# Optimization experiments

Hardware: AMD Instinct MI355X
Metric: run time of the kernel (lower is better)

## Reference

```python
import jax, jax.numpy as jnp
import numpy as np

SIGMA = 16.0


def setup_inputs() -> dict:
    key = jax.random.key(0)
    k1, k2, k3 = jax.random.split(key, 3)
    B, T, D = 8, 2048, 1024
    x = jax.random.normal(k1, (B, T, D), dtype=jnp.float32)
    posv = jax.random.randint(k2, (B, T), 0, 64, dtype=jnp.int32)
    posh = jax.random.randint(k3, (B, T), 0, 64, dtype=jnp.int32)
    return {"x": x, "posv": posv, "posh": posh}


def reference(x, posv, posh):
    # pos: [B, T, 2] float, as in torch.stack([posv, posh], -1).float()
    pos = jnp.stack([posv, posh], axis=-1).astype(jnp.float32)
    # pairwise squared distances: [B, T, T]
    diff = pos[:, :, None, :] - pos[:, None, :, :]
    dist_sq = jnp.sum(diff * diff, axis=-1)
    kernel = jnp.exp(-dist_sq / (2.0 * SIGMA * SIGMA))
    kernel = kernel / jnp.sum(kernel, axis=-1, keepdims=True)
    # dropout is identity in eval mode
    return jnp.einsum("bts,bsd->btd", kernel, x)
```

## Files before the change

kernel.cpp:

```cpp
#include <hip/hip_runtime.h>
#include <hip/hip_bf16.h>

#define NB 8
#define NT 2048
#define ND 1024
#define CAP 2048

typedef unsigned short ushort_t;
using short8 = __attribute__((ext_vector_type(8))) short;
using f32x4  = __attribute__((ext_vector_type(4))) float;

__device__ __forceinline__ ushort_t f2bf(float f) {
    __hip_bfloat16 h = __float2bfloat16(f);
    return *reinterpret_cast<ushort_t*>(&h);
}
__device__ __forceinline__ float bf2f(ushort_t u) {
    unsigned int v = ((unsigned int)u) << 16;
    return __int_as_float((int)v);
}

__device__ __forceinline__ int xcd_swizzle() {
    int bid = (int)blockIdx.x;
    return (bid >> 3) + ((bid & 7) * ((int)gridDim.x >> 3));
}


#define OFF_G2     256
#define OFF_AFH    768
#define OFF_AFL    8960
#define OFF_CNTV   17152
#define OFF_CNTH   19200
#define OFF_INVDEN 21248
#define OFF_GOFF   152320
#define OFF_TOKV   160512
#define OFF_TOKH   4354816
#define OFF_TOKV2  8549120
#define OFF_B1     12743424
#define B1_SLAB    ((size_t)64 * 64 * 1024 * 2)

__device__ __forceinline__ void kden_body(
    int kb, const int* __restrict__ posv, const int* __restrict__ posh,
    float* __restrict__ invden, int b0)
{
    int b   = b0 + (kb >> 3);
    int phg = kb & 7;
    int tid = threadIdx.x;

    __shared__ int   hist[64][64];
    __shared__ float g2s[128];
    __shared__ float tmp[64][8];

#pragma unroll
    for (int k = 0; k < 16; k++) ((int*)hist)[tid + (k << 8)] = 0;
    if (tid < 128) {
        int k = tid, r = k - 63;
        g2s[tid] = (k < 127) ? expf(-(float)(r * r) * (1.0f / 512.0f)) : 0.0f;
    }
    __syncthreads();
#pragma unroll
    for (int k = 0; k < 8; k++) {
        int t = (k << 8) + tid;
        atomicAdd(&hist[posv[b * NT + t]][posh[b * NT + t]], 1);
    }
    __syncthreads();
#pragma unroll
    for (int c = 0; c < 2; c++) {
        int cell = (c << 8) + tid;
        int j    = cell >> 3;
        int phl  = cell & 7;
        int ph   = (phg << 3) + phl;
        float s = 0.f;
        for (int k = 0; k < 64; k++)
            s += (float)hist[j][k] * g2s[63 + k - ph];
        tmp[j][phl] = s;
    }
    __syncthreads();
#pragma unroll
    for (int c = 0; c < 2; c++) {
        int cell = (c << 8) + tid;
        int pv   = cell >> 3;
        int phl  = cell & 7;
        int ph   = (phg << 3) + phl;
        float s = 0.f;
        for (int j = 0; j < 64; j++)
            s += g2s[63 + j - pv] * tmp[j][phl];
        invden[(b * 64 + pv) * 64 + ph] = 1.0f / s;
    }
}

__global__ __launch_bounds__(256) void k1_bucket(
    const int* __restrict__ posv, const int* __restrict__ posh,
    int* __restrict__ tokv2, int4* __restrict__ goff,
    int* __restrict__ tokh,
    int* __restrict__ cntv, int* __restrict__ cnth,
    float* __restrict__ gbase, ushort_t* __restrict__ AfH,
    ushort_t* __restrict__ AfL, float* __restrict__ invden, int nbkt)
{
    if ((int)blockIdx.x >= nbkt) {
        kden_body((int)blockIdx.x - nbkt, posv, posh, invden, 0);
        return;
    }

    int b    = blockIdx.x >> 5;
    int blk  = blockIdx.x & 31;
    int wave = threadIdx.x >> 6;
    int lane = threadIdx.x & 63;

    if (blockIdx.x == 0) {
        if (threadIdx.x < 192) {
            int k = (int)threadIdx.x - 64;
            float v = 0.0f;
            if (k >= 0 && k < 127) {
                int r = k - 63;
                v = expf(-(float)(r * r) * (1.0f / 512.0f));
            }
            gbase[threadIdx.x] = v;
        }
#pragma unroll
        for (int p = 0; p < 16; p++) {
            int pos = (p << 8) + (int)threadIdx.x;
            int i   = pos & 7;
            int ln  = (pos >> 3) & 63;
            int ks  = (pos >> 9) & 1;
            int w   = pos >> 10;
            int q   = (w << 4) + (ln & 15);
            int k   = (ks << 5) + ((i >> 2) << 4) + ((ln >> 4) << 2) + (i & 3);
            int dlt = q - k;
            float g = expf(-(float)(dlt * dlt) * (1.0f / 512.0f));
            ushort_t hi = f2bf(g);
            AfH[pos] = hi;
            AfL[pos] = f2bf(g - bf2f(hi));
        }
    }

    int task   = blk * 4 + wave;
    int bucket = task & 63;
    int use_ph = task >> 6;
    int bkt    = b * 64 + bucket;

    int comb[32];
#pragma unroll
    for (int k = 0; k < 32; k++) {
        int t = k * 64 + lane;
        comb[k] = posv[b * NT + t] | (posh[b * NT + t] << 16);
    }

    unsigned long long lmask = (1ull << lane) - 1ull;

    if (use_ph == 0) {
        int* dst = tokv2 + (size_t)bkt * CAP;
        int cg0 = 0, cg1 = 0, cg2 = 0, cg3 = 0;
#pragma unroll 4
        for (int k = 0; k < 32; k++) {
            bool hit = (comb[k] & 0xffff) == bucket;
            int grp = (comb[k] >> 20) & 3;
            cg0 += (int)__popcll(__ballot(hit && grp == 0));
            cg1 += (int)__popcll(__ballot(hit && grp == 1));
            cg2 += (int)__popcll(__ballot(hit && grp == 2));
            cg3 += (int)__popcll(__ballot(hit && grp == 3));
        }
        int s1 = cg0, s2 = cg0 + cg1, s3 = cg0 + cg1 + cg2;
        int tot = s3 + cg3;
        if (lane == 0) {
            goff[bkt] = make_int4(0, s1, s2, s3);
            cntv[bkt] = tot;
        }
        int c0 = 0, c1 = s1, c2 = s2, c3 = s3;
#pragma unroll 4
        for (int k = 0; k < 32; k++) {
            bool hit = (comb[k] & 0xffff) == bucket;
            int grp = (comb[k] >> 20) & 3;
            unsigned long long m0 = __ballot(hit && grp == 0);
            unsigned long long m1 = __ballot(hit && grp == 1);
            unsigned long long m2 = __ballot(hit && grp == 2);
            unsigned long long m3 = __ballot(hit && grp == 3);
            if (hit) {
                int p;
                if      (grp == 0) p = c0 + (int)__popcll(m0 & lmask);
                else if (grp == 1) p = c1 + (int)__popcll(m1 & lmask);
                else if (grp == 2) p = c2 + (int)__popcll(m2 & lmask);
                else               p = c3 + (int)__popcll(m3 & lmask);
                dst[p] = (k * 64 + lane) | (comb[k] & 0xffff0000);
            }
            c0 += (int)__popcll(m0); c1 += (int)__popcll(m1);
            c2 += (int)__popcll(m2); c3 += (int)__popcll(m3);
        }
    } else {
        int* dst = tokh + (size_t)bkt * CAP;
        int cursor = 0;
#pragma unroll 4
        for (int k = 0; k < 32; k++) {
            bool hit = ((comb[k] >> 16) == bucket);
            unsigned long long m = __ballot(hit);
            if (hit)
                dst[cursor + __popcll(m & lmask)] =
                    (k * 64 + lane) | ((comb[k] & 0xffff) << 16);
            cursor += (int)__popcll(m);
        }
        if (lane == 0) cnth[bkt] = cursor;
    }
}

__global__ __launch_bounds__(256) void kden(
    const int* __restrict__ posv, const int* __restrict__ posh,
    float* __restrict__ invden, int b0)
{
    kden_body((int)blockIdx.x, posv, posh, invden, b0);
}

__device__ __forceinline__ short8 ldsBfrag(const ushort_t* rowp, int ks, int g4) {
    const ushort_t* p = rowp + (ks << 5) + g4;
    uint2 lo = *(const uint2*)(p);
    uint2 hi = *(const uint2*)(p + 16);
    uint4 pk; pk.x = lo.x; pk.y = lo.y; pk.z = hi.x; pk.w = hi.y;
    return __builtin_bit_cast(short8, pk);
}

__global__ __launch_bounds__(256) void k2_convh(
    const float* __restrict__ x,
    const int* __restrict__ tokv2, const int* __restrict__ cntv,
    const int4* __restrict__ goff,
    const ushort_t* __restrict__ AfH, const ushort_t* __restrict__ AfL,
    ushort_t* __restrict__ B1, int b0)
{
    int ell  = xcd_swizzle();
    int dc   = ell & 15;
    int pv   = (ell >> 4) & 63;
    int b    = b0 + (ell >> 10);
    int tid  = threadIdx.x;
    int lane = tid & 63;
    int w    = tid >> 6;
    int d0   = dc << 6;

    __shared__ float ldsf[64 * 65];
    float    (*S)[65]   = (float(*)[65])ldsf;
    ushort_t (*S16)[68] = (ushort_t(*)[68])ldsf;

    int bucket = (b << 6) + pv;
    int n = cntv[bucket];
    const int* toks = tokv2 + (size_t)bucket * CAP;
    const float* xb = x + (((size_t)b * NT) << 10) + d0 + lane;

    int4 go = goff[bucket];
    int gs = (w == 0) ? go.x : (w == 1) ? go.y : (w == 2) ? go.z : go.w;
    int ge = (w == 3) ? n   : (w == 0) ? go.y : (w == 1) ? go.z : go.w;

    int wn0 = ge - gs; if (wn0 < 0) wn0 = 0; if (wn0 > 64) wn0 = 64;
    int m0  = wn0 > 8 ? 8 : wn0;
    int m1  = wn0 > 8 ? (wn0 > 16 ? 8 : wn0 - 8) : 0;
    int pkv = (wn0 > 0) ? toks[gs + lane] : 0;
    int pk0[8], pk1[8]; float xv0[8], xv1[8];
#pragma unroll
    for (int j = 0; j < 8; j++) pk0[j] = __builtin_amdgcn_readlane(pkv, j);
#pragma unroll
    for (int j = 0; j < 8; j++)
        if (j < m0) xv0[j] = xb[(size_t)(pk0[j] & 0xffff) << 10];
#pragma unroll
    for (int j = 0; j < 8; j++) pk1[j] = __builtin_amdgcn_readlane(pkv, 8 + j);
#pragma unroll
    for (int j = 0; j < 8; j++)
        if (j < m1) xv1[j] = xb[(size_t)(pk1[j] & 0xffff) << 10];

    short8 ahi[2], alo[2];
#pragma unroll
    for (int ks = 0; ks < 2; ks++) {
        int idx = ((((w << 1) + ks) << 6) + lane) << 3;
        ahi[ks] = *(const short8*)(AfH + idx);
        alo[ks] = *(const short8*)(AfL + idx);
    }

#pragma unroll
    for (int k = 0; k < 17; k++) {
        int idx = (k << 8) + tid;
        if (idx < 64 * 65) ldsf[idx] = 0.f;
    }
    __syncthreads();

#pragma unroll
    for (int j = 0; j < 8; j++)
        if (j < m0) S[lane][pk0[j] >> 16] += xv0[j];
#pragma unroll
    for (int j = 0; j < 8; j++)
        if (j < m1) S[lane][pk1[j] >> 16] += xv1[j];

    for (int i = 16; i < wn0; i += 8) {
        int m = wn0 - i; if (m > 8) m = 8;
        int pk[8]; float xv[8];
#pragma unroll
        for (int j = 0; j < 8; j++) pk[j] = __builtin_amdgcn_readlane(pkv, i + j);
#pragma unroll
        for (int j = 0; j < 8; j++)
            if (j < m) xv[j] = xb[(size_t)(pk[j] & 0xffff) << 10];
#pragma unroll
        for (int j = 0; j < 8; j++)
            if (j < m) S[lane][pk[j] >> 16] += xv[j];
    }
    for (int win = gs + 64; win < ge; win += 64) {
        int wn = ge - win; if (wn > 64) wn = 64;
        int pkw = toks[win + lane];
        for (int i = 0; i < wn; i += 8) {
            int m = wn - i; if (m > 8) m = 8;
            int pk[8]; float xv[8];
#pragma unroll
            for (int j = 0; j < 8; j++) pk[j] = __builtin_amdgcn_readlane(pkw, i + j);
#pragma unroll
            for (int j = 0; j < 8; j++)
                if (j < m) xv[j] = xb[(size_t)(pk[j] & 0xffff) << 10];
#pragma unroll
            for (int j = 0; j < 8; j++)
                if (j < m) S[lane][pk[j] >> 16] += xv[j];
        }
    }
    __syncthreads();

    {
        int r  = tid & 63;
        int c0 = (tid >> 6) << 4;
        float vals[16];
#pragma unroll
        for (int c = 0; c < 16; c++) vals[c] = S[r][c0 + c];
        __syncthreads();
#pragma unroll
        for (int c = 0; c < 16; c++) S16[r][c0 + c] = f2bf(vals[c]);
    }
    __syncthreads();

    int g4 = (lane >> 4) << 2;
    int qbase = (w << 4) + g4;

    f32x4 accs[4];
#pragma unroll
    for (int nt = 0; nt < 4; nt++) {
        const ushort_t* rowp = &S16[(nt << 4) + (lane & 15)][0];
        f32x4 a = {0.f, 0.f, 0.f, 0.f};
#pragma unroll
        for (int ks = 0; ks < 2; ks++) {
            short8 bf = ldsBfrag(rowp, ks, g4);
            a = __builtin_amdgcn_mfma_f32_16x16x32_bf16(ahi[ks], bf, a, 0, 0, 0);
            a = __builtin_amdgcn_mfma_f32_16x16x32_bf16(alo[ks], bf, a, 0, 0, 0);
        }
        accs[nt] = a;
    }
    __syncthreads();

#pragma unroll
    for (int nt = 0; nt < 4; nt++)
#pragma unroll
        for (int reg = 0; reg < 4; reg++)
            S16[qbase + reg][(nt << 4) + (lane & 15)] = f2bf(accs[nt][reg]);
    __syncthreads();

    ushort_t* B1p = B1 + (((size_t)(b - b0)) << 22) + (((size_t)pv) << 10) + d0;
#pragma unroll
    for (int pass = 0; pass < 2; pass++) {
        int row = (pass << 5) + (tid >> 3);
        int col = (tid & 7) << 3;
        uint4 v = *(const uint4*)(&S16[row][col]);
        *reinterpret_cast<uint4*>(B1p + ((size_t)row << 16) + col) = v;
    }
}

__global__ __launch_bounds__(256) void k3_convv(
    const int* __restrict__ tokh, const int* __restrict__ cnth,
    const ushort_t* __restrict__ AfH, const ushort_t* __restrict__ AfL,
    const ushort_t* __restrict__ B1, const float* __restrict__ invden,
    float* __restrict__ out, int b0)
{
    int ell  = xcd_swizzle();
    int dc   = ell & 15;
    int ph   = (ell >> 4) & 63;
    int b    = b0 + (ell >> 10);
    int tid  = threadIdx.x;
    int lane = tid & 63;
    int w    = tid >> 6;
    int d0   = dc << 6;

    int n = cnth[(b << 6) + ph];
    if (n == 0) return;

    __shared__ float ldsf[64 * 65];
    ushort_t (*u16)[68] = (ushort_t(*)[68])ldsf;
    float    (*y)[65]   = (float(*)[65])ldsf;

    const ushort_t* B1b = B1 + (((size_t)(b - b0)) << 22) + (((size_t)ph) << 16)
                        + d0 + lane;
#pragma unroll
    for (int it = 0; it < 16; it++) {
        int j = (w << 4) + it;
        u16[lane][j] = B1b[(size_t)j << 10];
    }
    __syncthreads();

    short8 ahi[2], alo[2];
#pragma unroll
    for (int ks = 0; ks < 2; ks++) {
        int idx = ((((w << 1) + ks) << 6) + lane) << 3;
        ahi[ks] = *(const short8*)(AfH + idx);
        alo[ks] = *(const short8*)(AfL + idx);
    }
    int g4 = (lane >> 4) << 2;
    int qbase = (w << 4) + g4;

    f32x4 accs[4];
#pragma unroll
    for (int nt = 0; nt < 4; nt++) {
        const ushort_t* rowp = &u16[(nt << 4) + (lane & 15)][0];
        f32x4 a = {0.f, 0.f, 0.f, 0.f};
#pragma unroll
        for (int ks = 0; ks < 2; ks++) {
            short8 bf = ldsBfrag(rowp, ks, g4);
            a = __builtin_amdgcn_mfma_f32_16x16x32_bf16(ahi[ks], bf, a, 0, 0, 0);
            a = __builtin_amdgcn_mfma_f32_16x16x32_bf16(alo[ks], bf, a, 0, 0, 0);
        }
        accs[nt] = a;
    }
    __syncthreads();

#pragma unroll
    for (int nt = 0; nt < 4; nt++)
#pragma unroll
        for (int reg = 0; reg < 4; reg++)
            y[qbase + reg][(nt << 4) + (lane & 15)] = accs[nt][reg];
    __syncthreads();

    const int* toks = tokh + ((size_t)((b << 6) + ph)) * CAP;
    float* outb = out + (((size_t)b * NT) << 10) + d0 + lane;
    const float* ivb = invden + ((b << 6) << 6) + ph;

    int nch = (n + 3) >> 2;
    for (int c = w; c < nch; c += 4) {
        int i0 = c << 2;
        int4 M = *(const int4*)(toks + i0);
        int pk[4];
        pk[0] = __builtin_amdgcn_readfirstlane(M.x);
        pk[1] = __builtin_amdgcn_readfirstlane(M.y);
        pk[2] = __builtin_amdgcn_readfirstlane(M.z);
        pk[3] = __builtin_amdgcn_readfirstlane(M.w);
#pragma unroll
        for (int j = 0; j < 4; j++) {
            if (i0 + j < n) {
                int t   = pk[j] & 0xffff;
                int pvt = pk[j] >> 16;
                float iv = ivb[pvt << 6];
                outb[(size_t)t << 10] = y[pvt][lane] * iv;
            }
        }
    }
}

__global__ __launch_bounds__(256) void k_naive(
    const float* __restrict__ x, const int* __restrict__ posv,
    const int* __restrict__ posh, float* __restrict__ out)
{
    int t   = blockIdx.x & (NT - 1);
    int b   = blockIdx.x >> 11;
    int tid = threadIdx.x;

    __shared__ float s_w[NT];
    __shared__ float s_red[256];

    int pvt = posv[b * NT + t];
    int pht = posh[b * NT + t];

    float dsum = 0.0f;
    for (int s = tid; s < NT; s += 256) {
        int dv = pvt - posv[b * NT + s];
        int dh = pht - posh[b * NT + s];
        float w = expf(-(float)(dv * dv + dh * dh) * (1.0f / 512.0f));
        s_w[s] = w;
        dsum += w;
    }
    s_red[tid] = dsum;
    __syncthreads();
    for (int off = 128; off > 0; off >>= 1) {
        if (tid < off) s_red[tid] += s_red[tid + off];
        __syncthreads();
    }
    float inv = 1.0f / s_red[0];

    float a0 = 0.f, a1 = 0.f, a2 = 0.f, a3 = 0.f;
    for (int s = 0; s < NT; s++) {
        float w = s_w[s];
        const float* xr = x + (((size_t)(b * NT + s)) << 10);
        a0 = fmaf(w, xr[tid + 0],   a0);
        a1 = fmaf(w, xr[tid + 256], a1);
        a2 = fmaf(w, xr[tid + 512], a2);
        a3 = fmaf(w, xr[tid + 768], a3);
    }
    size_t ob = (((size_t)(b * NT + t)) << 10) + tid;
    out[ob + 0]   = a0 * inv;
    out[ob + 256] = a1 * inv;
    out[ob + 512] = a2 * inv;
    out[ob + 768] = a3 * inv;
}

extern "C" void kernel_launch(void* const* d_in, const int* in_sizes, int n_in,
                              void* d_out, int out_size, void* d_ws, size_t ws_size,
                              hipStream_t stream) {
    const float* x    = (const float*)d_in[0];
    const int*   posv = (const int*)d_in[1];
    const int*   posh = (const int*)d_in[2];
    float*       out  = (float*)d_out;

    char* ws = (char*)d_ws;
    float*    gbase  = (float*)ws;
    ushort_t* AfH    = (ushort_t*)(ws + OFF_AFH);
    ushort_t* AfL    = (ushort_t*)(ws + OFF_AFL);
    int*      cntv   = (int*)(ws + OFF_CNTV);
    int*      cnth   = (int*)(ws + OFF_CNTH);
    float*    invden = (float*)(ws + OFF_INVDEN);
    int4*     goff   = (int4*)(ws + OFF_GOFF);
    int*      tokh   = (int*)(ws + OFF_TOKH);
    int*      tokv2  = (int*)(ws + OFF_TOKV2);
    ushort_t* B1     = (ushort_t*)(ws + OFF_B1);

    const size_t needFull = (size_t)OFF_B1 + (size_t)NB * B1_SLAB;
    const size_t needLoop = (size_t)OFF_B1 + B1_SLAB;

    if (ws_size >= needFull) {
        k1_bucket<<<NB * 32 + NB * 8, 256, 0, stream>>>(
            posv, posh, tokv2, goff, tokh, cntv, cnth, gbase, AfH, AfL,
            invden, NB * 32);
        k2_convh<<<NB * 1024, 256, 0, stream>>>(x, tokv2, cntv, goff, AfH, AfL, B1, 0);
        k3_convv<<<NB * 1024, 256, 0, stream>>>(tokh, cnth, AfH, AfL, B1, invden, out, 0);
    } else if (ws_size >= needLoop) {
        k1_bucket<<<NB * 32, 256, 0, stream>>>(
            posv, posh, tokv2, goff, tokh, cntv, cnth, gbase, AfH, AfL,
            invden, NB * 32);
        for (int b = 0; b < NB; b++) {
            kden<<<8, 256, 0, stream>>>(posv, posh, invden, b);
            k2_convh<<<1024, 256, 0, stream>>>(x, tokv2, cntv, goff, AfH, AfL, B1, b);
            k3_convv<<<1024, 256, 0, stream>>>(tokh, cnth, AfH, AfL, B1, invden, out, b);
        }
    } else {
        k_naive<<<NB * NT, 256, 0, stream>>>(x, posv, posh, out);
    }
}
```

Measured before the change: 72.07 us.

## Process two position buckets per k2_convh block with prefetch overlap

Each k2_convh block now handles two consecutive posv buckets instead of one, halving the grid. The first gather batch of the second bucket is issued before the first bucket's MFMA and store phase, so its global loads overlap with that work. This reuses the A-fragment loads across both buckets and cuts block launch overhead. In exchange there are fewer blocks to hide latency, more registers in use, and extra barriers inside each block.

```diff
diff --git a/kernel.cpp b/kernel.cpp
--- a/kernel.cpp
+++ b/kernel.cpp
@@ -225,8 +225,8 @@
 {
     int ell  = xcd_swizzle();
     int dc   = ell & 15;
-    int pv   = (ell >> 4) & 63;
-    int b    = b0 + (ell >> 10);
+    int pp   = (ell >> 4) & 31;
+    int b    = b0 + (ell >> 9);
     int tid  = threadIdx.x;
     int lane = tid & 63;
     int w    = tid >> 6;
@@ -236,30 +236,9 @@
     float    (*S)[65]   = (float(*)[65])ldsf;
     ushort_t (*S16)[68] = (ushort_t(*)[68])ldsf;
 
-    int bucket = (b << 6) + pv;
-    int n = cntv[bucket];
-    const int* toks = tokv2 + (size_t)bucket * CAP;
     const float* xb = x + (((size_t)b * NT) << 10) + d0 + lane;
 
-    int4 go = goff[bucket];
-    int gs = (w == 0) ? go.x : (w == 1) ? go.y : (w == 2) ? go.z : go.w;
-    int ge = (w == 3) ? n   : (w == 0) ? go.y : (w == 1) ? go.z : go.w;
-
-    int wn0 = ge - gs; if (wn0 < 0) wn0 = 0; if (wn0 > 64) wn0 = 64;
-    int m0  = wn0 > 8 ? 8 : wn0;
-    int m1  = wn0 > 8 ? (wn0 > 16 ? 8 : wn0 - 8) : 0;
-    int pkv = (wn0 > 0) ? toks[gs + lane] : 0;
-    int pk0[8], pk1[8]; float xv0[8], xv1[8];
-#pragma unroll
-    for (int j = 0; j < 8; j++) pk0[j] = __builtin_amdgcn_readlane(pkv, j);
-#pragma unroll
-    for (int j = 0; j < 8; j++)
-        if (j < m0) xv0[j] = xb[(size_t)(pk0[j] & 0xffff) << 10];
-#pragma unroll
-    for (int j = 0; j < 8; j++) pk1[j] = __builtin_amdgcn_readlane(pkv, 8 + j);
-#pragma unroll
-    for (int j = 0; j < 8; j++)
-        if (j < m1) xv1[j] = xb[(size_t)(pk1[j] & 0xffff) << 10];
+    int bucket0 = (b << 6) + (pp << 1);
 
     short8 ahi[2], alo[2];
 #pragma unroll
@@ -268,6 +247,29 @@
         ahi[ks] = *(const short8*)(AfH + idx);
         alo[ks] = *(const short8*)(AfL + idx);
     }
+    int g4 = (lane >> 4) << 2;
+    int qbase = (w << 4) + g4;
+
+    int n0 = cntv[bucket0];
+    const int* toks0 = tokv2 + (size_t)bucket0 * CAP;
+    int4 go0 = goff[bucket0];
+    int gs0 = (w == 0) ? go0.x : (w == 1) ? go0.y : (w == 2) ? go0.z : go0.w;
+    int ge0 = (w == 3) ? n0  : (w == 0) ? go0.y : (w == 1) ? go0.z : go0.w;
+    int wn0 = ge0 - gs0; if (wn0 < 0) wn0 = 0; if (wn0 > 64) wn0 = 64;
+    int m00 = wn0 > 8 ? 8 : wn0;
+    int m01 = wn0 > 8 ? (wn0 > 16 ? 8 : wn0 - 8) : 0;
+    int pkv0 = (wn0 > 0) ? toks0[gs0 + lane] : 0;
+    int pk00[8], pk01[8]; float xv00[8], xv01[8];
+#pragma unroll
+    for (int j = 0; j < 8; j++) pk00[j] = __builtin_amdgcn_readlane(pkv0, j);
+#pragma unroll
+    for (int j = 0; j < 8; j++)
+        if (j < m00) xv00[j] = xb[(size_t)(pk00[j] & 0xffff) << 10];
+#pragma unroll
+    for (int j = 0; j < 8; j++) pk01[j] = __builtin_amdgcn_readlane(pkv0, 8 + j);
+#pragma unroll
+    for (int j = 0; j < 8; j++)
+        if (j < m01) xv01[j] = xb[(size_t)(pk01[j] & 0xffff) << 10];
 
 #pragma unroll
     for (int k = 0; k < 17; k++) {
@@ -278,16 +280,15 @@
 
 #pragma unroll
     for (int j = 0; j < 8; j++)
-        if (j < m0) S[lane][pk0[j] >> 16] += xv0[j];
+        if (j < m00) S[lane][pk00[j] >> 16] += xv00[j];
 #pragma unroll
     for (int j = 0; j < 8; j++)
-        if (j < m1) S[lane][pk1[j] >> 16] += xv1[j];
-
+        if (j < m01) S[lane][pk01[j] >> 16] += xv01[j];
     for (int i = 16; i < wn0; i += 8) {
         int m = wn0 - i; if (m > 8) m = 8;
         int pk[8]; float xv[8];
 #pragma unroll
-        for (int j = 0; j < 8; j++) pk[j] = __builtin_amdgcn_readlane(pkv, i + j);
+        for (int j = 0; j < 8; j++) pk[j] = __builtin_amdgcn_readlane(pkv0, i + j);
 #pragma unroll
         for (int j = 0; j < 8; j++)
             if (j < m) xv[j] = xb[(size_t)(pk[j] & 0xffff) << 10];
@@ -295,9 +296,9 @@
         for (int j = 0; j < 8; j++)
             if (j < m) S[lane][pk[j] >> 16] += xv[j];
     }
-    for (int win = gs + 64; win < ge; win += 64) {
-        int wn = ge - win; if (wn > 64) wn = 64;
-        int pkw = toks[win + lane];
+    for (int win = gs0 + 64; win < ge0; win += 64) {
+        int wn = ge0 - win; if (wn > 64) wn = 64;
+        int pkw = toks0[win + lane];
         for (int i = 0; i < wn; i += 8) {
             int m = wn - i; if (m > 8) m = 8;
             int pk[8]; float xv[8];
@@ -311,6 +312,23 @@
                 if (j < m) S[lane][pk[j] >> 16] += xv[j];
         }
     }
+
+    int bucket1 = bucket0 + 1;
+    int n1 = cntv[bucket1];
+    const int* toks1 = tokv2 + (size_t)bucket1 * CAP;
+    int4 go1 = goff[bucket1];
+    int gs1 = (w == 0) ? go1.x : (w == 1) ? go1.y : (w == 2) ? go1.z : go1.w;
+    int ge1 = (w == 3) ? n1  : (w == 0) ? go1.y : (w == 1) ? go1.z : go1.w;
+    int wn1 = ge1 - gs1; if (wn1 < 0) wn1 = 0; if (wn1 > 64) wn1 = 64;
+    int m10 = wn1 > 8 ? 8 : wn1;
+    int pkv1 = (wn1 > 0) ? toks1[gs1 + lane] : 0;
+    int pk10[8]; float xv10[8];
+#pragma unroll
+    for (int j = 0; j < 8; j++) pk10[j] = __builtin_amdgcn_readlane(pkv1, j);
+#pragma unroll
+    for (int j = 0; j < 8; j++)
+        if (j < m10) xv10[j] = xb[(size_t)(pk10[j] & 0xffff) << 10];
+
     __syncthreads();
 
     {
@@ -325,38 +343,123 @@
     }
     __syncthreads();
 
-    int g4 = (lane >> 4) << 2;
-    int qbase = (w << 4) + g4;
-
-    f32x4 accs[4];
-#pragma unroll
-    for (int nt = 0; nt < 4; nt++) {
-        const ushort_t* rowp = &S16[(nt << 4) + (lane & 15)][0];
-        f32x4 a = {0.f, 0.f, 0.f, 0.f};
-#pragma unroll
-        for (int ks = 0; ks < 2; ks++) {
-            short8 bf = ldsBfrag(rowp, ks, g4);
-            a = __builtin_amdgcn_mfma_f32_16x16x32_bf16(ahi[ks], bf, a, 0, 0, 0);
-            a = __builtin_amdgcn_mfma_f32_16x16x32_bf16(alo[ks], bf, a, 0, 0, 0);
-        }
-        accs[nt] = a;
-    }
-    __syncthreads();
-
-#pragma unroll
-    for (int nt = 0; nt < 4; nt++)
-#pragma unroll
-        for (int reg = 0; reg < 4; reg++)
-            S16[qbase + reg][(nt << 4) + (lane & 15)] = f2bf(accs[nt][reg]);
-    __syncthreads();
-
-    ushort_t* B1p = B1 + (((size_t)(b - b0)) << 22) + (((size_t)pv) << 10) + d0;
-#pragma unroll
-    for (int pass = 0; pass < 2; pass++) {
-        int row = (pass << 5) + (tid >> 3);
-        int col = (tid & 7) << 3;
-        uint4 v = *(const uint4*)(&S16[row][col]);
-        *reinterpret_cast<uint4*>(B1p + ((size_t)row << 16) + col) = v;
+    {
+        f32x4 accs[4];
+#pragma unroll
+        for (int nt = 0; nt < 4; nt++) {
+            const ushort_t* rowp = &S16[(nt << 4) + (lane & 15)][0];
+            f32x4 a = {0.f, 0.f, 0.f, 0.f};
+#pragma unroll
+            for (int ks = 0; ks < 2; ks++) {
+                short8 bf = ldsBfrag(rowp, ks, g4);
+                a = __builtin_amdgcn_mfma_f32_16x16x32_bf16(ahi[ks], bf, a, 0, 0, 0);
+                a = __builtin_amdgcn_mfma_f32_16x16x32_bf16(alo[ks], bf, a, 0, 0, 0);
+            }
+            accs[nt] = a;
+        }
+        __syncthreads();
+#pragma unroll
+        for (int nt = 0; nt < 4; nt++)
+#pragma unroll
+            for (int reg = 0; reg < 4; reg++)
+                S16[qbase + reg][(nt << 4) + (lane & 15)] = f2bf(accs[nt][reg]);
+        __syncthreads();
+
+        ushort_t* B1p = B1 + (((size_t)(b - b0)) << 22)
+                      + (((size_t)(pp << 1)) << 10) + d0;
+#pragma unroll
+        for (int pass = 0; pass < 2; pass++) {
+            int row = (pass << 5) + (tid >> 3);
+            int col = (tid & 7) << 3;
+            uint4 v = *(const uint4*)(&S16[row][col]);
+            *reinterpret_cast<uint4*>(B1p + ((size_t)row << 16) + col) = v;
+        }
+    }
+    __syncthreads();
+
+#pragma unroll
+    for (int k = 0; k < 17; k++) {
+        int idx = (k << 8) + tid;
+        if (idx < 64 * 65) ldsf[idx] = 0.f;
+    }
+    __syncthreads();
+
+#pragma unroll
+    for (int j = 0; j < 8; j++)
+        if (j < m10) S[lane][pk10[j] >> 16] += xv10[j];
+    for (int i = 8; i < wn1; i += 8) {
+        int m = wn1 - i; if (m > 8) m = 8;
+        int pk[8]; float xv[8];
+#pragma unroll
+        for (int j = 0; j < 8; j++) pk[j] = __builtin_amdgcn_readlane(pkv1, i + j);
+#pragma unroll
+        for (int j = 0; j < 8; j++)
+            if (j < m) xv[j] = xb[(size_t)(pk[j] & 0xffff) << 10];
+#pragma unroll
+        for (int j = 0; j < 8; j++)
+            if (j < m) S[lane][pk[j] >> 16] += xv[j];
+    }
+    for (int win = gs1 + 64; win < ge1; win += 64) {
+        int wn = ge1 - win; if (wn > 64) wn = 64;
+        int pkw = toks1[win + lane];
+        for (int i = 0; i < wn; i += 8) {
+            int m = wn - i; if (m > 8) m = 8;
+            int pk[8]; float xv[8];
+#pragma unroll
+            for (int j = 0; j < 8; j++) pk[j] = __builtin_amdgcn_readlane(pkw, i + j);
+#pragma unroll
+            for (int j = 0; j < 8; j++)
+                if (j < m) xv[j] = xb[(size_t)(pk[j] & 0xffff) << 10];
+#pragma unroll
+            for (int j = 0; j < 8; j++)
+                if (j < m) S[lane][pk[j] >> 16] += xv[j];
+        }
+    }
+    __syncthreads();
+
+    {
+        int r  = tid & 63;
+        int c0 = (tid >> 6) << 4;
+        float vals[16];
+#pragma unroll
+        for (int c = 0; c < 16; c++) vals[c] = S[r][c0 + c];
+        __syncthreads();
+#pragma unroll
+        for (int c = 0; c < 16; c++) S16[r][c0 + c] = f2bf(vals[c]);
+    }
+    __syncthreads();
+
+    {
+        f32x4 accs[4];
+#pragma unroll
+        for (int nt = 0; nt < 4; nt++) {
+            const ushort_t* rowp = &S16[(nt << 4) + (lane & 15)][0];
+            f32x4 a = {0.f, 0.f, 0.f, 0.f};
+#pragma unroll
+            for (int ks = 0; ks < 2; ks++) {
+                short8 bf = ldsBfrag(rowp, ks, g4);
+                a = __builtin_amdgcn_mfma_f32_16x16x32_bf16(ahi[ks], bf, a, 0, 0, 0);
+                a = __builtin_amdgcn_mfma_f32_16x16x32_bf16(alo[ks], bf, a, 0, 0, 0);
+            }
+            accs[nt] = a;
+        }
+        __syncthreads();
+#pragma unroll
+        for (int nt = 0; nt < 4; nt++)
+#pragma unroll
+            for (int reg = 0; reg < 4; reg++)
+                S16[qbase + reg][(nt << 4) + (lane & 15)] = f2bf(accs[nt][reg]);
+        __syncthreads();
+
+        ushort_t* B1p = B1 + (((size_t)(b - b0)) << 22)
+                      + (((size_t)((pp << 1) + 1)) << 10) + d0;
+#pragma unroll
+        for (int pass = 0; pass < 2; pass++) {
+            int row = (pass << 5) + (tid >> 3);
+            int col = (tid & 7) << 3;
+            uint4 v = *(const uint4*)(&S16[row][col]);
+            *reinterpret_cast<uint4*>(B1p + ((size_t)row << 16) + col) = v;
+        }
     }
 }
 
@@ -521,7 +624,7 @@
         k1_bucket<<<NB * 32 + NB * 8, 256, 0, stream>>>(
             posv, posh, tokv2, goff, tokh, cntv, cnth, gbase, AfH, AfL,
             invden, NB * 32);
-        k2_convh<<<NB * 1024, 256, 0, stream>>>(x, tokv2, cntv, goff, AfH, AfL, B1, 0);
+        k2_convh<<<NB * 512, 256, 0, stream>>>(x, tokv2, cntv, goff, AfH, AfL, B1, 0);
         k3_convv<<<NB * 1024, 256, 0, stream>>>(tokh, cnth, AfH, AfL, B1, invden, out, 0);
     } else if (ws_size >= needLoop) {
         k1_bucket<<<NB * 32, 256, 0, stream>>>(
@@ -529,7 +632,7 @@
             invden, NB * 32);
         for (int b = 0; b < NB; b++) {
             kden<<<8, 256, 0, stream>>>(posv, posh, invden, b);
-            k2_convh<<<1024, 256, 0, stream>>>(x, tokv2, cntv, goff, AfH, AfL, B1, b);
+            k2_convh<<<512, 256, 0, stream>>>(x, tokv2, cntv, goff, AfH, AfL, B1, b);
             k3_convv<<<1024, 256, 0, stream>>>(tokh, cnth, AfH, AfL, B1, invden, out, b);
         }
     } else {
```

Result: slower. 75.40 us (+4.6%).
